# Kernel tuning notes

Measured on AMD Instinct MI355X. Metric: run time of the kernel, lower is better.

The kernel has to match this reference:

```python
import jax, jax.numpy as jnp
import numpy as np

B, S, N_WIRES, EMBED_DIM, NUM_HEADS = 4, 2048, 8, 512, 8
D_K = EMBED_DIM // NUM_HEADS


def setup_inputs() -> dict:
    key = jax.random.key(0)
    k_x, k_th, k_q, k_k, k_v, k_c = jax.random.split(key, 6)
    x = jax.random.normal(k_x, (B, S, N_WIRES), dtype=jnp.float32)
    # trainable RX rotation angles, one per wire
    theta = jax.random.normal(k_th, (N_WIRES,), dtype=jnp.float32) * 0.1
    # nn.Linear(n_wires, embed_dim, bias=False) weights have shape (embed_dim, n_wires)
    sc_in = 1.0 / np.sqrt(N_WIRES)
    Wq = jax.random.normal(k_q, (EMBED_DIM, N_WIRES), dtype=jnp.float32) * sc_in
    Wk = jax.random.normal(k_k, (EMBED_DIM, N_WIRES), dtype=jnp.float32) * sc_in
    Wv = jax.random.normal(k_v, (EMBED_DIM, N_WIRES), dtype=jnp.float32) * sc_in
    Wc = jax.random.normal(k_c, (EMBED_DIM, EMBED_DIM), dtype=jnp.float32) * (1.0 / np.sqrt(EMBED_DIM))
    return {"x": x, "theta": theta, "Wq": Wq, "Wk": Wk, "Wv": Wv, "Wc": Wc}


def reference(x, theta, Wq, Wk, Wv, Wc):
    # Quantum encoding closed form: RX(x_i) then RX(theta_i) on |0> per wire gives <Z> = cos(x_i + theta_i).
    proj = jnp.cos(x + theta)  # (B, S, n_wires)
    b, s, _ = proj.shape
    q = jnp.einsum('bsn,en->bse', proj, Wq)
    k = jnp.einsum('bsn,en->bse', proj, Wk)
    v = jnp.einsum('bsn,en->bse', proj, Wv)
    # split heads: (B, H, S, d_k)
    q = q.reshape(b, s, NUM_HEADS, D_K).transpose(0, 2, 1, 3)
    k = k.reshape(b, s, NUM_HEADS, D_K).transpose(0, 2, 1, 3)
    v = v.reshape(b, s, NUM_HEADS, D_K).transpose(0, 2, 1, 3)
    scores = jnp.einsum('bhqd,bhkd->bhqk', q, k) / np.sqrt(D_K).astype(np.float32)
    attn = jax.nn.softmax(scores, axis=-1)  # dropout is identity at inference
    out = jnp.einsum('bhqk,bhkd->bhqd', attn, v)
    out = out.transpose(0, 2, 1, 3).reshape(b, s, EMBED_DIM)
    return jnp.einsum('bse,fe->bsf', out, Wc)
```

## Files before the change

### kernel.cpp

```cpp
#include <hip/hip_runtime.h>
#include <stdint.h>

#define N_B 4
#define S_LEN 2048
#define N_H 8
#define E_DIM 512

typedef __attribute__((ext_vector_type(8))) short bf16x8;
typedef __attribute__((ext_vector_type(4))) float f32x4;
typedef __attribute__((ext_vector_type(4))) unsigned int u32x4;
typedef __attribute__((ext_vector_type(2))) unsigned int u32x2;
typedef __attribute__((ext_vector_type(4))) unsigned short u16x4;
typedef __attribute__((ext_vector_type(8))) unsigned short u16x8;

#define MFMA16(a, b, c) __builtin_amdgcn_mfma_f32_16x16x32_bf16((a), (b), (c), 0, 0, 0)

#define LSTR 68

__device__ __forceinline__ unsigned short f2bf(float f) {
    union { float f; unsigned int u; } v; v.f = f;
    unsigned int r = v.u + 0x7fffu + ((v.u >> 16) & 1u);
    return (unsigned short)(r >> 16);
}

__device__ __forceinline__ unsigned int pack2bf(float lo, float hi) {
    union { float f; unsigned int u; } a, b; a.f = lo; b.f = hi;
    return __builtin_amdgcn_perm(b.u + 0x8000u, a.u + 0x8000u, 0x07060302u);
}

__device__ __forceinline__ float fexp2(float x) {
#if __has_builtin(__builtin_amdgcn_exp2f)
    return __builtin_amdgcn_exp2f(x);
#else
    return exp2f(x);
#endif
}

#define Q_SCALE 0.18033688f

__global__ __launch_bounds__(256) void qkv_kernel(
    const float* __restrict__ x, const float* __restrict__ theta,
    const float* __restrict__ Wq, const float* __restrict__ Wk,
    const float* __restrict__ Wv,
    unsigned short* __restrict__ Q, unsigned short* __restrict__ K,
    unsigned short* __restrict__ Vt)
{
    __shared__ float proj[32][8];
    const int tid = threadIdx.x;
    const int mat = blockIdx.x % 3;
    const int chunk = blockIdx.x / 3;
    const int row0 = chunk * 32;
    const int b = row0 >> 11;
    const int s_in_b = row0 & (S_LEN - 1);

    proj[tid >> 3][tid & 7] = cosf(x[row0 * 8 + tid] + theta[tid & 7]);
    __syncthreads();

    if (mat < 2) {
        const float* W = (mat == 0) ? Wq : Wk;
        const float scale = (mat == 0) ? Q_SCALE : 1.0f;
        unsigned short* outp = (mat == 0) ? Q : K;
        const int eg = (tid & 127) * 4;
        const int sg = (tid >> 7) * 16;
        float w[4][8];
        #pragma unroll
        for (int e = 0; e < 4; ++e)
            #pragma unroll
            for (int n = 0; n < 8; ++n)
                w[e][n] = W[(eg + e) * 8 + n] * scale;
        const int h = eg >> 6, d0 = eg & 63;
        unsigned short* p0 = outp + ((size_t)(b * N_H + h) * S_LEN + s_in_b + sg) * 64 + d0;
        #pragma unroll 4
        for (int s = 0; s < 16; ++s) {
            f32x4 pa = *(const f32x4*)&proj[sg + s][0];
            f32x4 pc = *(const f32x4*)&proj[sg + s][4];
            u16x4 o;
            #pragma unroll
            for (int e = 0; e < 4; ++e) {
                float a = 0.f;
                #pragma unroll
                for (int n = 0; n < 4; ++n)
                    a += pa[n] * w[e][n] + pc[n] * w[e][n + 4];
                o[e] = f2bf(a);
            }
            *(u16x4*)&p0[s * 64] = o;
        }
    } else {
        f32x4 ps[8][2];
        const int sl0 = (tid & 3) * 8;
        #pragma unroll
        for (int k2 = 0; k2 < 8; ++k2) {
            ps[k2][0] = *(const f32x4*)&proj[sl0 + k2][0];
            ps[k2][1] = *(const f32x4*)&proj[sl0 + k2][4];
        }
        const int ecol = tid >> 2;
        for (int pass = 0; pass < 8; ++pass) {
            const int e = pass * 64 + ecol;
            const int h = e >> 6, dd = e & 63;
            float wr[8];
            #pragma unroll
            for (int n = 0; n < 8; ++n) wr[n] = Wv[e * 8 + n];
            u16x8 pk;
            #pragma unroll
            for (int k2 = 0; k2 < 8; ++k2) {
                float acc = 0.f;
                #pragma unroll
                for (int n = 0; n < 4; ++n)
                    acc += ps[k2][0][n] * wr[n] + ps[k2][1][n] * wr[n + 4];
                pk[k2] = f2bf(acc);
            }
            *(u16x8*)&Vt[((size_t)(b * N_H + h) * 64 + dd) * S_LEN + s_in_b + sl0] = pk;
        }
    }
}

__global__ __launch_bounds__(128, 2) void flash_kernel(
    const unsigned short* __restrict__ Q, const unsigned short* __restrict__ K,
    const unsigned short* __restrict__ Vt,
    float* __restrict__ OP, float* __restrict__ LS)
{
    __shared__ short kt[64 * LSTR];
    __shared__ short vt[64 * LSTR];
    __shared__ short pb[128 * LSTR];

    const int tid = threadIdx.x;
    const int lane = tid & 63, w = tid >> 6;
    const int quad = lane >> 4, lq = lane & 15;
    const int kh = blockIdx.x & 1;
    const int qt = (blockIdx.x >> 1) & 15;
    const int bh = blockIdx.x >> 5;

    const unsigned short* Qb = Q + (size_t)bh * S_LEN * 64;
    const unsigned short* Kb = K + ((size_t)bh * S_LEN + kh * 1024) * 64;
    const unsigned short* Vb = Vt + (size_t)bh * 64 * S_LEN + kh * 1024;

    bf16x8 qf[4][2];
    #pragma unroll
    for (int mt = 0; mt < 4; ++mt)
        #pragma unroll
        for (int ks = 0; ks < 2; ++ks)
            qf[mt][ks] = *(const bf16x8*)&Qb[(size_t)(qt * 128 + w * 64 + mt * 16 + lq) * 64 + ks * 32 + quad * 8];

    f32x4 oacc[4][4];
    #pragma unroll
    for (int mt = 0; mt < 4; ++mt)
        #pragma unroll
        for (int dt = 0; dt < 4; ++dt) oacc[mt][dt] = 0.f;
    float lsum[4] = {0.f, 0.f, 0.f, 0.f};

    u32x4 pkr[4], pvr[4];
    #pragma unroll
    for (int i = 0; i < 4; ++i) {
        const int u = tid + (i << 7);
        pkr[i] = *(const u32x4*)&Kb[(size_t)(u >> 3) * 64 + (u & 7) * 8];
        pvr[i] = *(const u32x4*)&Vb[(size_t)(u >> 3) * S_LEN + (u & 7) * 8];
    }

    for (int kti = 0; kti < 16; ++kti) {
        __syncthreads();
        #pragma unroll
        for (int i = 0; i < 4; ++i) {
            const int u = tid + (i << 7);
            *(u32x4*)&kt[(u >> 3) * LSTR + (u & 7) * 8] = pkr[i];
            *(u32x4*)&vt[(u >> 3) * LSTR + (u & 7) * 8] = pvr[i];
        }
        __syncthreads();

        const int kb2 = (kti < 15) ? (kti + 1) * 64 : 0;
        #pragma unroll
        for (int i = 0; i < 4; ++i) {
            const int u = tid + (i << 7);
            pkr[i] = *(const u32x4*)&Kb[(size_t)(kb2 + (u >> 3)) * 64 + (u & 7) * 8];
            pvr[i] = *(const u32x4*)&Vb[(size_t)(u >> 3) * S_LEN + kb2 + (u & 7) * 8];
        }

        f32x4 sacc[4][4];
        #pragma unroll
        for (int mt = 0; mt < 4; ++mt)
            #pragma unroll
            for (int mts = 0; mts < 4; ++mts) sacc[mt][mts] = 0.f;
        #pragma unroll
        for (int mts = 0; mts < 4; ++mts) {
            #pragma unroll
            for (int ks = 0; ks < 2; ++ks) {
                bf16x8 af = *(const bf16x8*)&kt[(mts * 16 + lq) * LSTR + ks * 32 + quad * 8];
                #pragma unroll
                for (int mt = 0; mt < 4; ++mt)
                    sacc[mt][mts] = MFMA16(af, qf[mt][ks], sacc[mt][mts]);
            }
        }

        #pragma unroll
        for (int mt = 0; mt < 4; ++mt) {
            #pragma unroll
            for (int mts = 0; mts < 4; ++mts) {
                f32x4 p;
                #pragma unroll
                for (int e = 0; e < 4; ++e) p[e] = fexp2(sacc[mt][mts][e]);
                lsum[mt] += (p[0] + p[1]) + (p[2] + p[3]);
                u32x2 pw = { pack2bf(p[0], p[1]), pack2bf(p[2], p[3]) };
                *(u32x2*)&pb[(w * 64 + mt * 16 + lq) * LSTR + mts * 16 + quad * 4] = pw;
            }
        }

        #pragma unroll
        for (int ks = 0; ks < 2; ++ks) {
            bf16x8 af[4];
            #pragma unroll
            for (int mt = 0; mt < 4; ++mt)
                af[mt] = *(const bf16x8*)&pb[(w * 64 + mt * 16 + lq) * LSTR + ks * 32 + quad * 8];
            #pragma unroll
            for (int dt = 0; dt < 4; ++dt) {
                bf16x8 bf = *(const bf16x8*)&vt[(dt * 16 + lq) * LSTR + ks * 32 + quad * 8];
                #pragma unroll
                for (int mt = 0; mt < 4; ++mt)
                    oacc[mt][dt] = MFMA16(af[mt], bf, oacc[mt][dt]);
            }
        }
    }

    float* OPb = OP + ((size_t)(kh * 32 + bh) * S_LEN + qt * 128) * 64;
    float* LSb = LS + ((size_t)(kh * 32 + bh) * S_LEN + qt * 128);
    #pragma unroll
    for (int mt = 0; mt < 4; ++mt) {
        float rs = lsum[mt];
        rs += __shfl_xor(rs, 16);
        rs += __shfl_xor(rs, 32);
        if (quad == 0) LSb[w * 64 + mt * 16 + lq] = rs;
        #pragma unroll
        for (int dt = 0; dt < 4; ++dt)
            #pragma unroll
            for (int r = 0; r < 4; ++r)
                OPb[(size_t)(w * 64 + mt * 16 + quad * 4 + r) * 64 + dt * 16 + lq] = oacc[mt][dt][r];
    }
}

__global__ __launch_bounds__(256) void combine_kernel(
    const float* __restrict__ OP, const float* __restrict__ LS,
    unsigned short* __restrict__ O)
{
    const int t = blockIdx.x * 256 + threadIdx.x;
    const int bhq = t >> 2;
    const int dg = (t & 3) << 4;
    const int bh = bhq >> 11, q = bhq & 2047;
    const int b = bh >> 3, h = bh & 7;
    const float ls = LS[(size_t)bh * S_LEN + q] + LS[(size_t)(32 + bh) * S_LEN + q];
    const float inv = 1.0f / ls;
    const float* p0 = OP + ((size_t)bh * S_LEN + q) * 64 + dg;
    const float* p1 = OP + ((size_t)(32 + bh) * S_LEN + q) * 64 + dg;
    unsigned short* dst = O + ((size_t)b * S_LEN + q) * E_DIM + h * 64 + dg;
    #pragma unroll
    for (int c = 0; c < 4; ++c) {
        f32x4 a = *(const f32x4*)&p0[c * 4];
        f32x4 bb = *(const f32x4*)&p1[c * 4];
        u16x4 o = { f2bf((a[0] + bb[0]) * inv), f2bf((a[1] + bb[1]) * inv),
                    f2bf((a[2] + bb[2]) * inv), f2bf((a[3] + bb[3]) * inv) };
        *(u16x4*)&dst[c * 4] = o;
    }
}

__global__ __launch_bounds__(256, 4) void outproj_kernel(
    const unsigned short* __restrict__ O, const float* __restrict__ Wc,
    float* __restrict__ Y)
{
    __shared__ short at[64 * LSTR];
    __shared__ short bt[64 * LSTR];
    const int tid = threadIdx.x;
    const int lane = tid & 63, w = tid >> 6;
    const int quad = lane >> 4, lq = lane & 15;
    const int m0 = (blockIdx.x >> 3) * 64;
    const int f0 = (blockIdx.x & 7) * 64;

    f32x4 acc[4];
    #pragma unroll
    for (int nt = 0; nt < 4; ++nt) acc[nt] = 0.f;

    u32x4 pa[2];
    f32x4 pw[4];
    #pragma unroll
    for (int i = 0; i < 2; ++i) {
        const int u = tid + (i << 8);
        pa[i] = *(const u32x4*)&O[(size_t)(m0 + (u >> 3)) * E_DIM + (u & 7) * 8];
    }
    #pragma unroll
    for (int i = 0; i < 4; ++i) {
        const int u = tid + (i << 8);
        pw[i] = *(const f32x4*)&Wc[(size_t)(f0 + (u >> 4)) * E_DIM + (u & 15) * 4];
    }

    for (int e0 = 0; e0 < E_DIM; e0 += 64) {
        __syncthreads();
        #pragma unroll
        for (int i = 0; i < 2; ++i) {
            const int u = tid + (i << 8);
            *(u32x4*)&at[(u >> 3) * LSTR + (u & 7) * 8] = pa[i];
        }
        #pragma unroll
        for (int i = 0; i < 4; ++i) {
            const int u = tid + (i << 8);
            u16x4 pk = { f2bf(pw[i][0]), f2bf(pw[i][1]), f2bf(pw[i][2]), f2bf(pw[i][3]) };
            *(u16x4*)&bt[(u >> 4) * LSTR + (u & 15) * 4] = pk;
        }
        __syncthreads();

        const int e1 = (e0 + 64 < E_DIM) ? e0 + 64 : 0;
        #pragma unroll
        for (int i = 0; i < 2; ++i) {
            const int u = tid + (i << 8);
            pa[i] = *(const u32x4*)&O[(size_t)(m0 + (u >> 3)) * E_DIM + e1 + (u & 7) * 8];
        }
        #pragma unroll
        for (int i = 0; i < 4; ++i) {
            const int u = tid + (i << 8);
            pw[i] = *(const f32x4*)&Wc[(size_t)(f0 + (u >> 4)) * E_DIM + e1 + (u & 15) * 4];
        }

        bf16x8 afk[2];
        #pragma unroll
        for (int ks = 0; ks < 2; ++ks)
            afk[ks] = *(const bf16x8*)&at[(w * 16 + lq) * LSTR + ks * 32 + quad * 8];
        #pragma unroll
        for (int nt = 0; nt < 4; ++nt) {
            #pragma unroll
            for (int ks = 0; ks < 2; ++ks) {
                bf16x8 bf = *(const bf16x8*)&bt[(nt * 16 + lq) * LSTR + ks * 32 + quad * 8];
                acc[nt] = MFMA16(afk[ks], bf, acc[nt]);
            }
        }
    }

    #pragma unroll
    for (int nt = 0; nt < 4; ++nt)
        #pragma unroll
        for (int r = 0; r < 4; ++r)
            Y[(size_t)(m0 + w * 16 + quad * 4 + r) * E_DIM + f0 + nt * 16 + lq] = acc[nt][r];
}

extern "C" void kernel_launch(void* const* d_in, const int* in_sizes, int n_in,
                              void* d_out, int out_size, void* d_ws, size_t ws_size,
                              hipStream_t stream) {
    const float* x     = (const float*)d_in[0];
    const float* theta = (const float*)d_in[1];
    const float* Wq    = (const float*)d_in[2];
    const float* Wk    = (const float*)d_in[3];
    const float* Wv    = (const float*)d_in[4];
    const float* Wc    = (const float*)d_in[5];
    float* Y = (float*)d_out;

    char* ws = (char*)d_ws;
    unsigned short* Q  = (unsigned short*)(ws);
    unsigned short* K  = (unsigned short*)(ws + ((size_t)8 << 20));
    unsigned short* Vt = (unsigned short*)(ws + ((size_t)16 << 20));
    float*          OP = (float*)(ws + ((size_t)24 << 20));
    float*          LS = (float*)(ws + ((size_t)56 << 20));
    unsigned short* O  = Q;

    qkv_kernel<<<(N_B * S_LEN / 32) * 3, 256, 0, stream>>>(x, theta, Wq, Wk, Wv, Q, K, Vt);
    flash_kernel<<<N_B * N_H * (S_LEN / 128) * 2, 128, 0, stream>>>(Q, K, Vt, OP, LS);
    combine_kernel<<<(N_B * N_H * S_LEN * 4) / 256, 256, 0, stream>>>(OP, LS, O);
    outproj_kernel<<<(N_B * S_LEN / 64) * (E_DIM / 64), 256, 0, stream>>>(O, Wc, Y);
}
```

Before: 144.3 us.

## Split keys four ways, store bf16 partials, fuse combine into out-projection

The flash kernel now splits the key range into four chunks instead of two, which doubles the grid and raises the occupancy hint. V fragments are loaded straight from global memory into registers with a one-tile prefetch, so V no longer goes through shared memory. Partial outputs are stored as bf16 rather than fp32, and the separate combine kernel is removed. Its sum-and-normalise step now runs while the out-projection loads its A tiles, which cuts one launch and reduces workspace traffic, at the cost of an extra bf16 rounding on the partials and redundant combine work repeated across the eight f-tiles.

```diff
diff --git a/kernel.cpp b/kernel.cpp
--- a/kernel.cpp
+++ b/kernel.cpp
@@ -21,6 +21,11 @@
     union { float f; unsigned int u; } v; v.f = f;
     unsigned int r = v.u + 0x7fffu + ((v.u >> 16) & 1u);
     return (unsigned short)(r >> 16);
+}
+
+__device__ __forceinline__ float bf2f(unsigned short u) {
+    union { unsigned int u; float f; } v; v.u = (unsigned int)u << 16;
+    return v.f;
 }
 
 __device__ __forceinline__ unsigned int pack2bf(float lo, float hi) {
@@ -114,25 +119,24 @@
     }
 }
 
-__global__ __launch_bounds__(128, 2) void flash_kernel(
+__global__ __launch_bounds__(128, 3) void flash_kernel(
     const unsigned short* __restrict__ Q, const unsigned short* __restrict__ K,
     const unsigned short* __restrict__ Vt,
-    float* __restrict__ OP, float* __restrict__ LS)
+    unsigned short* __restrict__ OP, float* __restrict__ LS)
 {
     __shared__ short kt[64 * LSTR];
-    __shared__ short vt[64 * LSTR];
     __shared__ short pb[128 * LSTR];
 
     const int tid = threadIdx.x;
     const int lane = tid & 63, w = tid >> 6;
     const int quad = lane >> 4, lq = lane & 15;
-    const int kh = blockIdx.x & 1;
-    const int qt = (blockIdx.x >> 1) & 15;
-    const int bh = blockIdx.x >> 5;
+    const int kh = blockIdx.x & 3;
+    const int qt = (blockIdx.x >> 2) & 15;
+    const int bh = blockIdx.x >> 6;
 
     const unsigned short* Qb = Q + (size_t)bh * S_LEN * 64;
-    const unsigned short* Kb = K + ((size_t)bh * S_LEN + kh * 1024) * 64;
-    const unsigned short* Vb = Vt + (size_t)bh * 64 * S_LEN + kh * 1024;
+    const unsigned short* Kb = K + ((size_t)bh * S_LEN + kh * 512) * 64;
+    const unsigned short* Vb = Vt + (size_t)bh * 64 * S_LEN + kh * 512;
 
     bf16x8 qf[4][2];
     #pragma unroll
@@ -148,31 +152,39 @@
         for (int dt = 0; dt < 4; ++dt) oacc[mt][dt] = 0.f;
     float lsum[4] = {0.f, 0.f, 0.f, 0.f};
 
-    u32x4 pkr[4], pvr[4];
+    u32x4 pkr[4];
+    bf16x8 vf[2][4], vfn[2][4];
     #pragma unroll
     for (int i = 0; i < 4; ++i) {
         const int u = tid + (i << 7);
         pkr[i] = *(const u32x4*)&Kb[(size_t)(u >> 3) * 64 + (u & 7) * 8];
-        pvr[i] = *(const u32x4*)&Vb[(size_t)(u >> 3) * S_LEN + (u & 7) * 8];
-    }
-
-    for (int kti = 0; kti < 16; ++kti) {
+    }
+    #pragma unroll
+    for (int ks = 0; ks < 2; ++ks)
+        #pragma unroll
+        for (int dt = 0; dt < 4; ++dt)
+            vf[ks][dt] = *(const bf16x8*)&Vb[(size_t)(dt * 16 + lq) * S_LEN + ks * 32 + quad * 8];
+
+    for (int kti = 0; kti < 8; ++kti) {
         __syncthreads();
         #pragma unroll
         for (int i = 0; i < 4; ++i) {
             const int u = tid + (i << 7);
             *(u32x4*)&kt[(u >> 3) * LSTR + (u & 7) * 8] = pkr[i];
-            *(u32x4*)&vt[(u >> 3) * LSTR + (u & 7) * 8] = pvr[i];
         }
         __syncthreads();
 
-        const int kb2 = (kti < 15) ? (kti + 1) * 64 : 0;
+        const int kb2 = (kti < 7) ? (kti + 1) * 64 : 0;
         #pragma unroll
         for (int i = 0; i < 4; ++i) {
             const int u = tid + (i << 7);
             pkr[i] = *(const u32x4*)&Kb[(size_t)(kb2 + (u >> 3)) * 64 + (u & 7) * 8];
-            pvr[i] = *(const u32x4*)&Vb[(size_t)(u >> 3) * S_LEN + kb2 + (u & 7) * 8];
-        }
+        }
+        #pragma unroll
+        for (int ks = 0; ks < 2; ++ks)
+            #pragma unroll
+            for (int dt = 0; dt < 4; ++dt)
+                vfn[ks][dt] = *(const bf16x8*)&Vb[(size_t)(dt * 16 + lq) * S_LEN + kb2 + ks * 32 + quad * 8];
 
         f32x4 sacc[4][4];
         #pragma unroll
@@ -211,16 +223,20 @@
                 af[mt] = *(const bf16x8*)&pb[(w * 64 + mt * 16 + lq) * LSTR + ks * 32 + quad * 8];
             #pragma unroll
             for (int dt = 0; dt < 4; ++dt) {
-                bf16x8 bf = *(const bf16x8*)&vt[(dt * 16 + lq) * LSTR + ks * 32 + quad * 8];
                 #pragma unroll
                 for (int mt = 0; mt < 4; ++mt)
-                    oacc[mt][dt] = MFMA16(af[mt], bf, oacc[mt][dt]);
-            }
-        }
-    }
-
-    float* OPb = OP + ((size_t)(kh * 32 + bh) * S_LEN + qt * 128) * 64;
-    float* LSb = LS + ((size_t)(kh * 32 + bh) * S_LEN + qt * 128);
+                    oacc[mt][dt] = MFMA16(af[mt], vf[ks][dt], oacc[mt][dt]);
+            }
+        }
+        #pragma unroll
+        for (int ks = 0; ks < 2; ++ks)
+            #pragma unroll
+            for (int dt = 0; dt < 4; ++dt)
+                vf[ks][dt] = vfn[ks][dt];
+    }
+
+    unsigned short* OPb = OP + ((size_t)(kh * 32 + bh) * S_LEN + qt * 128) * 64;
+    float* LSb = LS + (size_t)(kh * 32 + bh) * S_LEN + qt * 128;
     #pragma unroll
     for (int mt = 0; mt < 4; ++mt) {
         float rs = lsum[mt];
@@ -231,37 +247,13 @@
         for (int dt = 0; dt < 4; ++dt)
             #pragma unroll
             for (int r = 0; r < 4; ++r)
-                OPb[(size_t)(w * 64 + mt * 16 + quad * 4 + r) * 64 + dt * 16 + lq] = oacc[mt][dt][r];
-    }
-}
-
-__global__ __launch_bounds__(256) void combine_kernel(
-    const float* __restrict__ OP, const float* __restrict__ LS,
-    unsigned short* __restrict__ O)
-{
-    const int t = blockIdx.x * 256 + threadIdx.x;
-    const int bhq = t >> 2;
-    const int dg = (t & 3) << 4;
-    const int bh = bhq >> 11, q = bhq & 2047;
-    const int b = bh >> 3, h = bh & 7;
-    const float ls = LS[(size_t)bh * S_LEN + q] + LS[(size_t)(32 + bh) * S_LEN + q];
-    const float inv = 1.0f / ls;
-    const float* p0 = OP + ((size_t)bh * S_LEN + q) * 64 + dg;
-    const float* p1 = OP + ((size_t)(32 + bh) * S_LEN + q) * 64 + dg;
-    unsigned short* dst = O + ((size_t)b * S_LEN + q) * E_DIM + h * 64 + dg;
-    #pragma unroll
-    for (int c = 0; c < 4; ++c) {
-        f32x4 a = *(const f32x4*)&p0[c * 4];
-        f32x4 bb = *(const f32x4*)&p1[c * 4];
-        u16x4 o = { f2bf((a[0] + bb[0]) * inv), f2bf((a[1] + bb[1]) * inv),
-                    f2bf((a[2] + bb[2]) * inv), f2bf((a[3] + bb[3]) * inv) };
-        *(u16x4*)&dst[c * 4] = o;
-    }
-}
-
-__global__ __launch_bounds__(256, 4) void outproj_kernel(
-    const unsigned short* __restrict__ O, const float* __restrict__ Wc,
-    float* __restrict__ Y)
+                OPb[(size_t)(w * 64 + mt * 16 + quad * 4 + r) * 64 + dt * 16 + lq] = f2bf(oacc[mt][dt][r]);
+    }
+}
+
+__global__ __launch_bounds__(256) void outproj_kernel(
+    const unsigned short* __restrict__ OP, const float* __restrict__ LS,
+    const float* __restrict__ Wc, float* __restrict__ Y)
 {
     __shared__ short at[64 * LSTR];
     __shared__ short bt[64 * LSTR];
@@ -275,12 +267,21 @@
     #pragma unroll
     for (int nt = 0; nt < 4; ++nt) acc[nt] = 0.f;
 
-    u32x4 pa[2];
+    u16x8 pA[2][4];
+    float pls[2];
     f32x4 pw[4];
+
     #pragma unroll
     for (int i = 0; i < 2; ++i) {
         const int u = tid + (i << 8);
-        pa[i] = *(const u32x4*)&O[(size_t)(m0 + (u >> 3)) * E_DIM + (u & 7) * 8];
+        const int r = u >> 3, c8 = (u & 7) * 8;
+        const int m = m0 + r, b = m >> 11, s = m & (S_LEN - 1);
+        const int bi = b * 8 + 0;
+        pls[i] = LS[(size_t)bi * S_LEN + s] + LS[(size_t)(bi + 32) * S_LEN + s]
+               + LS[(size_t)(bi + 64) * S_LEN + s] + LS[(size_t)(bi + 96) * S_LEN + s];
+        #pragma unroll
+        for (int kh = 0; kh < 4; ++kh)
+            pA[i][kh] = *(const u16x8*)&OP[((size_t)(kh * 32 + bi) * S_LEN + s) * 64 + c8];
     }
     #pragma unroll
     for (int i = 0; i < 4; ++i) {
@@ -288,12 +289,21 @@
         pw[i] = *(const f32x4*)&Wc[(size_t)(f0 + (u >> 4)) * E_DIM + (u & 15) * 4];
     }
 
-    for (int e0 = 0; e0 < E_DIM; e0 += 64) {
+    for (int c = 0; c < 8; ++c) {
         __syncthreads();
         #pragma unroll
         for (int i = 0; i < 2; ++i) {
             const int u = tid + (i << 8);
-            *(u32x4*)&at[(u >> 3) * LSTR + (u & 7) * 8] = pa[i];
+            const int r = u >> 3, c8 = (u & 7) * 8;
+            const float inv = __builtin_amdgcn_rcpf(pls[i]);
+            u16x8 o;
+            #pragma unroll
+            for (int e = 0; e < 8; ++e) {
+                float v = bf2f(pA[i][0][e]) + bf2f(pA[i][1][e])
+                        + bf2f(pA[i][2][e]) + bf2f(pA[i][3][e]);
+                o[e] = f2bf(v * inv);
+            }
+            *(u16x8*)&at[r * LSTR + c8] = o;
         }
         #pragma unroll
         for (int i = 0; i < 4; ++i) {
@@ -303,16 +313,23 @@
         }
         __syncthreads();
 
-        const int e1 = (e0 + 64 < E_DIM) ? e0 + 64 : 0;
+        const int cn = (c < 7) ? c + 1 : 0;
         #pragma unroll
         for (int i = 0; i < 2; ++i) {
             const int u = tid + (i << 8);
-            pa[i] = *(const u32x4*)&O[(size_t)(m0 + (u >> 3)) * E_DIM + e1 + (u & 7) * 8];
+            const int r = u >> 3, c8 = (u & 7) * 8;
+            const int m = m0 + r, b = m >> 11, s = m & (S_LEN - 1);
+            const int bi = b * 8 + cn;
+            pls[i] = LS[(size_t)bi * S_LEN + s] + LS[(size_t)(bi + 32) * S_LEN + s]
+                   + LS[(size_t)(bi + 64) * S_LEN + s] + LS[(size_t)(bi + 96) * S_LEN + s];
+            #pragma unroll
+            for (int kh = 0; kh < 4; ++kh)
+                pA[i][kh] = *(const u16x8*)&OP[((size_t)(kh * 32 + bi) * S_LEN + s) * 64 + c8];
         }
         #pragma unroll
         for (int i = 0; i < 4; ++i) {
             const int u = tid + (i << 8);
-            pw[i] = *(const f32x4*)&Wc[(size_t)(f0 + (u >> 4)) * E_DIM + e1 + (u & 15) * 4];
+            pw[i] = *(const f32x4*)&Wc[(size_t)(f0 + (u >> 4)) * E_DIM + cn * 64 + (u & 15) * 4];
         }
 
         bf16x8 afk[2];
@@ -351,12 +368,10 @@
     unsigned short* Q  = (unsigned short*)(ws);
     unsigned short* K  = (unsigned short*)(ws + ((size_t)8 << 20));
     unsigned short* Vt = (unsigned short*)(ws + ((size_t)16 << 20));
-    float*          OP = (float*)(ws + ((size_t)24 << 20));
+    unsigned short* OP = (unsigned short*)(ws + ((size_t)24 << 20));
     float*          LS = (float*)(ws + ((size_t)56 << 20));
-    unsigned short* O  = Q;
 
     qkv_kernel<<<(N_B * S_LEN / 32) * 3, 256, 0, stream>>>(x, theta, Wq, Wk, Wv, Q, K, Vt);
-    flash_kernel<<<N_B * N_H * (S_LEN / 128) * 2, 128, 0, stream>>>(Q, K, Vt, OP, LS);
-    combine_kernel<<<(N_B * N_H * S_LEN * 4) / 256, 256, 0, stream>>>(OP, LS, O);
-    outproj_kernel<<<(N_B * S_LEN / 64) * (E_DIM / 64), 256, 0, stream>>>(O, Wc, Y);
-}
+    flash_kernel<<<N_B * N_H * (S_LEN / 128) * 4, 128, 0, stream>>>(Q, K, Vt, OP, LS);
+    outproj_kernel<<<(N_B * S_LEN / 64) * (E_DIM / 64), 256, 0, stream>>>(OP, LS, Wc, Y);
+}
```

New measurement: 348.0 us. 2.41x slower.

## Split attention keys four ways, store bf16 partials, and halve P scratch

Applied to the files above, without the earlier changes.

The flash kernel now splits each head's key range into four 512-key chunks instead of two, doubling the grid to give more blocks for occupancy. Partial outputs are written as bf16 instead of fp32 so the extra partials do not double write and read traffic, and the combine kernel sums four partials. The P scratch tile in shared memory is halved by processing the exp/pack and PV MFMA steps in two passes of 32 rows, which may raise occupancy. Rounding each partial to bf16 before combining adds some precision loss.

```diff
diff --git a/kernel.cpp b/kernel.cpp
--- a/kernel.cpp
+++ b/kernel.cpp
@@ -21,6 +21,11 @@
     union { float f; unsigned int u; } v; v.f = f;
     unsigned int r = v.u + 0x7fffu + ((v.u >> 16) & 1u);
     return (unsigned short)(r >> 16);
+}
+
+__device__ __forceinline__ float bf2f(unsigned short u) {
+    union { unsigned int u; float f; } v; v.u = (unsigned int)u << 16;
+    return v.f;
 }
 
 __device__ __forceinline__ unsigned int pack2bf(float lo, float hi) {
@@ -117,22 +122,22 @@
 __global__ __launch_bounds__(128, 2) void flash_kernel(
     const unsigned short* __restrict__ Q, const unsigned short* __restrict__ K,
     const unsigned short* __restrict__ Vt,
-    float* __restrict__ OP, float* __restrict__ LS)
+    unsigned short* __restrict__ OP, float* __restrict__ LS)
 {
     __shared__ short kt[64 * LSTR];
     __shared__ short vt[64 * LSTR];
-    __shared__ short pb[128 * LSTR];
+    __shared__ short pb[64 * LSTR];
 
     const int tid = threadIdx.x;
     const int lane = tid & 63, w = tid >> 6;
     const int quad = lane >> 4, lq = lane & 15;
-    const int kh = blockIdx.x & 1;
-    const int qt = (blockIdx.x >> 1) & 15;
-    const int bh = blockIdx.x >> 5;
+    const int kh = blockIdx.x & 3;
+    const int qt = (blockIdx.x >> 2) & 15;
+    const int bh = blockIdx.x >> 6;
 
     const unsigned short* Qb = Q + (size_t)bh * S_LEN * 64;
-    const unsigned short* Kb = K + ((size_t)bh * S_LEN + kh * 1024) * 64;
-    const unsigned short* Vb = Vt + (size_t)bh * 64 * S_LEN + kh * 1024;
+    const unsigned short* Kb = K + ((size_t)bh * S_LEN + kh * 512) * 64;
+    const unsigned short* Vb = Vt + (size_t)bh * 64 * S_LEN + kh * 512;
 
     bf16x8 qf[4][2];
     #pragma unroll
@@ -156,7 +161,7 @@
         pvr[i] = *(const u32x4*)&Vb[(size_t)(u >> 3) * S_LEN + (u & 7) * 8];
     }
 
-    for (int kti = 0; kti < 16; ++kti) {
+    for (int kti = 0; kti < 8; ++kti) {
         __syncthreads();
         #pragma unroll
         for (int i = 0; i < 4; ++i) {
@@ -166,7 +171,7 @@
         }
         __syncthreads();
 
-        const int kb2 = (kti < 15) ? (kti + 1) * 64 : 0;
+        const int kb2 = (kti < 7) ? (kti + 1) * 64 : 0;
         #pragma unroll
         for (int i = 0; i < 4; ++i) {
             const int u = tid + (i << 7);
@@ -191,36 +196,36 @@
         }
 
         #pragma unroll
-        for (int mt = 0; mt < 4; ++mt) {
-            #pragma unroll
-            for (int mts = 0; mts < 4; ++mts) {
-                f32x4 p;
-                #pragma unroll
-                for (int e = 0; e < 4; ++e) p[e] = fexp2(sacc[mt][mts][e]);
-                lsum[mt] += (p[0] + p[1]) + (p[2] + p[3]);
-                u32x2 pw = { pack2bf(p[0], p[1]), pack2bf(p[2], p[3]) };
-                *(u32x2*)&pb[(w * 64 + mt * 16 + lq) * LSTR + mts * 16 + quad * 4] = pw;
-            }
-        }
-
-        #pragma unroll
-        for (int ks = 0; ks < 2; ++ks) {
-            bf16x8 af[4];
-            #pragma unroll
-            for (int mt = 0; mt < 4; ++mt)
-                af[mt] = *(const bf16x8*)&pb[(w * 64 + mt * 16 + lq) * LSTR + ks * 32 + quad * 8];
-            #pragma unroll
-            for (int dt = 0; dt < 4; ++dt) {
-                bf16x8 bf = *(const bf16x8*)&vt[(dt * 16 + lq) * LSTR + ks * 32 + quad * 8];
-                #pragma unroll
-                for (int mt = 0; mt < 4; ++mt)
-                    oacc[mt][dt] = MFMA16(af[mt], bf, oacc[mt][dt]);
-            }
-        }
-    }
-
-    float* OPb = OP + ((size_t)(kh * 32 + bh) * S_LEN + qt * 128) * 64;
-    float* LSb = LS + ((size_t)(kh * 32 + bh) * S_LEN + qt * 128);
+        for (int mtp = 0; mtp < 2; ++mtp) {
+            #pragma unroll
+            for (int mtl = 0; mtl < 2; ++mtl) {
+                const int mt = mtp * 2 + mtl;
+                #pragma unroll
+                for (int mts = 0; mts < 4; ++mts) {
+                    f32x4 p;
+                    #pragma unroll
+                    for (int e = 0; e < 4; ++e) p[e] = fexp2(sacc[mt][mts][e]);
+                    lsum[mt] += (p[0] + p[1]) + (p[2] + p[3]);
+                    u32x2 pw = { pack2bf(p[0], p[1]), pack2bf(p[2], p[3]) };
+                    *(u32x2*)&pb[(w * 32 + mtl * 16 + lq) * LSTR + mts * 16 + quad * 4] = pw;
+                }
+            }
+            #pragma unroll
+            for (int ks = 0; ks < 2; ++ks) {
+                bf16x8 af0 = *(const bf16x8*)&pb[(w * 32 + lq) * LSTR + ks * 32 + quad * 8];
+                bf16x8 af1 = *(const bf16x8*)&pb[(w * 32 + 16 + lq) * LSTR + ks * 32 + quad * 8];
+                #pragma unroll
+                for (int dt = 0; dt < 4; ++dt) {
+                    bf16x8 bf = *(const bf16x8*)&vt[(dt * 16 + lq) * LSTR + ks * 32 + quad * 8];
+                    oacc[mtp * 2 + 0][dt] = MFMA16(af0, bf, oacc[mtp * 2 + 0][dt]);
+                    oacc[mtp * 2 + 1][dt] = MFMA16(af1, bf, oacc[mtp * 2 + 1][dt]);
+                }
+            }
+        }
+    }
+
+    unsigned short* OPb = OP + ((size_t)(kh * 32 + bh) * S_LEN + qt * 128) * 64;
+    float* LSb = LS + (size_t)(kh * 32 + bh) * S_LEN + qt * 128;
     #pragma unroll
     for (int mt = 0; mt < 4; ++mt) {
         float rs = lsum[mt];
@@ -231,12 +236,12 @@
         for (int dt = 0; dt < 4; ++dt)
             #pragma unroll
             for (int r = 0; r < 4; ++r)
-                OPb[(size_t)(w * 64 + mt * 16 + quad * 4 + r) * 64 + dt * 16 + lq] = oacc[mt][dt][r];
+                OPb[(size_t)(w * 64 + mt * 16 + quad * 4 + r) * 64 + dt * 16 + lq] = f2bf(oacc[mt][dt][r]);
     }
 }
 
 __global__ __launch_bounds__(256) void combine_kernel(
-    const float* __restrict__ OP, const float* __restrict__ LS,
+    const unsigned short* __restrict__ OP, const float* __restrict__ LS,
     unsigned short* __restrict__ O)
 {
     const int t = blockIdx.x * 256 + threadIdx.x;
@@ -244,18 +249,29 @@
     const int dg = (t & 3) << 4;
     const int bh = bhq >> 11, q = bhq & 2047;
     const int b = bh >> 3, h = bh & 7;
-    const float ls = LS[(size_t)bh * S_LEN + q] + LS[(size_t)(32 + bh) * S_LEN + q];
+    float ls = 0.f;
+    #pragma unroll
+    for (int kh = 0; kh < 4; ++kh)
+        ls += LS[(size_t)(kh * 32 + bh) * S_LEN + q];
     const float inv = 1.0f / ls;
-    const float* p0 = OP + ((size_t)bh * S_LEN + q) * 64 + dg;
-    const float* p1 = OP + ((size_t)(32 + bh) * S_LEN + q) * 64 + dg;
+    u16x8 pp[4][2];
+    #pragma unroll
+    for (int kh = 0; kh < 4; ++kh) {
+        const unsigned short* p = &OP[((size_t)(kh * 32 + bh) * S_LEN + q) * 64 + dg];
+        pp[kh][0] = *(const u16x8*)&p[0];
+        pp[kh][1] = *(const u16x8*)&p[8];
+    }
     unsigned short* dst = O + ((size_t)b * S_LEN + q) * E_DIM + h * 64 + dg;
     #pragma unroll
-    for (int c = 0; c < 4; ++c) {
-        f32x4 a = *(const f32x4*)&p0[c * 4];
-        f32x4 bb = *(const f32x4*)&p1[c * 4];
-        u16x4 o = { f2bf((a[0] + bb[0]) * inv), f2bf((a[1] + bb[1]) * inv),
-                    f2bf((a[2] + bb[2]) * inv), f2bf((a[3] + bb[3]) * inv) };
-        *(u16x4*)&dst[c * 4] = o;
+    for (int c = 0; c < 2; ++c) {
+        u16x8 o;
+        #pragma unroll
+        for (int e = 0; e < 8; ++e) {
+            float v = bf2f(pp[0][c][e]) + bf2f(pp[1][c][e])
+                    + bf2f(pp[2][c][e]) + bf2f(pp[3][c][e]);
+            o[e] = f2bf(v * inv);
+        }
+        *(u16x8*)&dst[c * 8] = o;
     }
 }
 
@@ -351,12 +367,12 @@
     unsigned short* Q  = (unsigned short*)(ws);
     unsigned short* K  = (unsigned short*)(ws + ((size_t)8 << 20));
     unsigned short* Vt = (unsigned short*)(ws + ((size_t)16 << 20));
-    float*          OP = (float*)(ws + ((size_t)24 << 20));
+    unsigned short* OP = (unsigned short*)(ws + ((size_t)24 << 20));
     float*          LS = (float*)(ws + ((size_t)56 << 20));
     unsigned short* O  = Q;
 
     qkv_kernel<<<(N_B * S_LEN / 32) * 3, 256, 0, stream>>>(x, theta, Wq, Wk, Wv, Q, K, Vt);
-    flash_kernel<<<N_B * N_H * (S_LEN / 128) * 2, 128, 0, stream>>>(Q, K, Vt, OP, LS);
+    flash_kernel<<<N_B * N_H * (S_LEN / 128) * 4, 128, 0, stream>>>(Q, K, Vt, OP, LS);
     combine_kernel<<<(N_B * N_H * S_LEN * 4) / 256, 256, 0, stream>>>(OP, LS, O);
     outproj_kernel<<<(N_B * S_LEN / 64) * (E_DIM / 64), 256, 0, stream>>>(O, Wc, Y);
 }
```

New measurement: 150.5 us. +4.3%, slower.
